# Kernel tuning notes

Measured on AMD Instinct MI355X. Metric: run time of the kernel, lower is better.

Reference implementation:

```python
import jax, jax.numpy as jnp
import numpy as np

N = 100000          # num nodes
E = 1600000         # num edges (before self loops)
IN_C = 128
OUT_C = 64
RATIO = 0.5
NEG_SLOPE = 0.2


def setup_inputs() -> dict:
    key = jax.random.key(0)
    k1, k2, k3, k4, k5 = jax.random.split(key, 5)
    x = jax.random.normal(k1, (N, IN_C), jnp.float32)
    # edges with no self loops (module removes then re-adds self loops)
    src = jax.random.randint(k2, (E,), 0, N, dtype=jnp.int32)
    off = jax.random.randint(k3, (E,), 1, N, dtype=jnp.int32)
    tgt = (src + off) % N
    edge_index = jnp.stack([src, tgt])  # [2, E], row0=source(j), row1=target(i)
    # glorot init
    s_w = float(np.sqrt(6.0 / (IN_C + OUT_C)))
    weight = jax.random.uniform(k4, (IN_C, OUT_C), jnp.float32, -s_w, s_w)
    s_a = float(np.sqrt(6.0 / (1 + 2 * OUT_C)))
    att = jax.random.uniform(k5, (1, 2 * OUT_C), jnp.float32, -s_a, s_a)
    batch = jnp.zeros((N,), jnp.int32)  # single graph
    return {"x": x, "weight": weight, "att": att,
            "edge_index": edge_index, "batch": batch, "bn": 0}


def reference(x, weight, att, edge_index, batch, bn):
    # add self loops (static shapes: E + N edges)
    loops = jnp.arange(N, dtype=edge_index.dtype)
    src = jnp.concatenate([edge_index[0], loops])  # edge_index_j (source)
    tgt = jnp.concatenate([edge_index[1], loops])  # edge_index_i (target)

    h = x @ weight                      # [N, OUT_C]
    x_j = h[src]                        # [E+N, OUT_C] gathered source feats
    x_i = h[tgt]

    # alpha = (cat([x_i, x_j]) * att).sum(-1)
    alpha = x_i @ att[0, :OUT_C] + x_j @ att[0, OUT_C:]   # [E+N]
    alpha = jnp.where(alpha > 0, alpha, NEG_SLOPE * alpha)  # leaky_relu

    # edge-softmax grouped by target node (every node has a self loop -> no empty segment)
    m = jax.ops.segment_max(alpha, tgt, num_segments=N)
    a = jnp.exp(alpha - m[tgt])
    denom = jax.ops.segment_sum(a, tgt, num_segments=N)
    alpha = a / (denom[tgt] + 1e-16)

    # node importance = sum of attention over outgoing edges (grouped by source)
    alpha_sum = jax.ops.segment_sum(alpha, src, num_segments=N)

    # topk node selection (ratio of all nodes; single graph)
    k = int(np.ceil(RATIO * N))
    _, topk_idx = jax.lax.top_k(alpha_sum, k)
    node_mask = jnp.zeros((N,), bool).at[topk_idx].set(True)

    # filter_dn: keep edges whose both endpoints survive; mask instead of compacting
    edge_mask = node_mask[src] & node_mask[tgt]
    alpha_m = jnp.where(edge_mask, alpha, 0.0)

    # weighted scatter-add aggregation to target nodes (aggr='add')
    out = jax.ops.segment_sum(alpha_m[:, None] * x_j, tgt, num_segments=N)  # [N, OUT_C]
    # bn flag is 0 -> BatchNorm skipped
    return out, edge_mask, node_mask
```

## Files before the change

kernel.cpp:

```cpp
#include <hip/hip_runtime.h>
#include <stdint.h>

#define IN_C 128
#define OUT_C 64
#define NEG_SLOPE 0.2f
#define RB 256
#define RBINS 512
#define STAGE 8192
#define NGH (RBINS * RB)
#define NGHS (RBINS * RBINS)
#define KC 8
#define SXW 384

typedef unsigned int u32;
typedef unsigned long long u64;

__device__ __forceinline__ u32 fenc(float f) {
  u32 u = __float_as_uint(f);
  return (u & 0x80000000u) ? ~u : (u | 0x80000000u);
}
__device__ __forceinline__ u64 key64(float v, int i) {
  return (((u64)fenc(v)) << 32) | (u64)(0xffffffffu - (u32)i);
}

__global__ __launch_bounds__(256) void k_gemm(const float* __restrict__ x,
                                              const float* __restrict__ w,
                                              const float* __restrict__ att,
                                              float* __restrict__ h,
                                              float* __restrict__ ai, float* __restrict__ aj,
                                              int N) {
  __shared__ float sw[IN_C * OUT_C];
  __shared__ float sx[KC * SXW];
  int tid = threadIdx.x;
  int rbase = blockIdx.x * 256;

  for (int i = tid; i < (IN_C * OUT_C) / 4; i += 256)
    ((float4*)sw)[i] = ((const float4*)w)[i];

  int c0 = (tid & 7) * 8;
  int rg = tid >> 3;
  int sxbase = rg * 12;
  float acc[8][8];
#pragma unroll
  for (int i = 0; i < 8; i++)
#pragma unroll
    for (int j = 0; j < 8; j++) acc[i][j] = 0.f;

  int str = tid >> 1;
  int skq = tid & 1;

  for (int kb = 0; kb < IN_C; kb += KC) {
    __syncthreads();
#pragma unroll
    for (int it = 0; it < 2; ++it) {
      int r = str + it * 128;
      int grow = rbase + r;
      float4 v = make_float4(0.f, 0.f, 0.f, 0.f);
      if (grow < N) v = *(const float4*)&x[(size_t)grow * IN_C + kb + skq * 4];
      int base = (r >> 3) * 12 + (r & 7);
      sx[(skq * 4 + 0) * SXW + base] = v.x;
      sx[(skq * 4 + 1) * SXW + base] = v.y;
      sx[(skq * 4 + 2) * SXW + base] = v.z;
      sx[(skq * 4 + 3) * SXW + base] = v.w;
    }
    __syncthreads();
#pragma unroll
    for (int kl = 0; kl < KC; ++kl) {
      int kg = kb + kl;
      float xr[8], wv[8];
      *(float4*)&xr[0] = *(const float4*)&sx[kl * SXW + sxbase];
      *(float4*)&xr[4] = *(const float4*)&sx[kl * SXW + sxbase + 4];
      *(float4*)&wv[0] = *(const float4*)&sw[kg * OUT_C + c0];
      *(float4*)&wv[4] = *(const float4*)&sw[kg * OUT_C + c0 + 4];
#pragma unroll
      for (int i = 0; i < 8; ++i)
#pragma unroll
        for (int j = 0; j < 8; ++j)
          acc[i][j] += xr[i] * wv[j];
    }
  }

  float pi[8], pj[8];
#pragma unroll
  for (int i = 0; i < 8; ++i) { pi[i] = 0.f; pj[i] = 0.f; }
#pragma unroll
  for (int j = 0; j < 8; ++j) {
    float a0 = att[c0 + j], a1 = att[OUT_C + c0 + j];
#pragma unroll
    for (int i = 0; i < 8; ++i) {
      pi[i] += acc[i][j] * a0;
      pj[i] += acc[i][j] * a1;
    }
  }
#pragma unroll
  for (int o = 1; o < 8; o <<= 1) {
#pragma unroll
    for (int i = 0; i < 8; ++i) {
      pi[i] += __shfl_xor(pi[i], o);
      pj[i] += __shfl_xor(pj[i], o);
    }
  }
#pragma unroll
  for (int i = 0; i < 8; ++i) {
    int row = rbase + rg * 8 + i;
    if (row < N) {
      *(float4*)&h[(size_t)row * OUT_C + c0]     = make_float4(acc[i][0], acc[i][1], acc[i][2], acc[i][3]);
      *(float4*)&h[(size_t)row * OUT_C + c0 + 4] = make_float4(acc[i][4], acc[i][5], acc[i][6], acc[i][7]);
      if ((tid & 7) == 0) { ai[row] = pi[i]; aj[row] = pj[i]; }
    }
  }
}

__global__ __launch_bounds__(256) void k_rhist_t(const int* __restrict__ tgt,
                                                 int E, int EN, int chunk, u32* __restrict__ gh,
                                                 u32* __restrict__ hist8, u32* __restrict__ done,
                                                 u32* __restrict__ sel, u32* __restrict__ cnt, u32 k) {
  __shared__ u32 lh[RBINS];
  int tid = threadIdx.x, b = blockIdx.x;
  if (b == 0) {
    for (int i = tid; i < 2048; i += 256) hist8[i] = 0u;
    if (tid < 8) { done[tid] = 0u; cnt[tid] = 0u; }
    if (tid == 0) { sel[0] = 0u; sel[1] = 0u; sel[2] = k; sel[3] = 0u; }
  }
  for (int d = tid; d < RBINS; d += 256) lh[d] = 0u;
  __syncthreads();
  int lo = b * chunk, hi = min(lo + chunk, EN);
  for (int e = lo + tid; e < hi; e += 256) {
    int t = (e < E) ? tgt[e] : e - E;
    atomicAdd(&lh[((u32)t) >> 8], 1u);
  }
  __syncthreads();
  for (int d = tid; d < RBINS; d += 256) gh[d * RB + b] = lh[d];
}

__global__ __launch_bounds__(256) void k_scanA(const u32* __restrict__ in, u32* __restrict__ out,
                                               u32* __restrict__ bsum, int n) {
  __shared__ u32 s[256];
  int i = blockIdx.x * 256 + threadIdx.x;
  u32 v = (i < n) ? in[i] : 0u;
  s[threadIdx.x] = v;
  __syncthreads();
  for (int o = 1; o < 256; o <<= 1) {
    u32 t = (threadIdx.x >= (unsigned)o) ? s[threadIdx.x - o] : 0u;
    __syncthreads();
    s[threadIdx.x] += t;
    __syncthreads();
  }
  if (i < n) out[i] = s[threadIdx.x] - v;
  if (threadIdx.x == 255) bsum[blockIdx.x] = s[255];
}

__global__ __launch_bounds__(1024) void k_scanB(u32* __restrict__ bsum, int nb) {
  __shared__ u32 s[1024];
  int tid = threadIdx.x;
  u32 v = (tid < nb) ? bsum[tid] : 0u;
  s[tid] = v;
  __syncthreads();
  for (int o = 1; o < 1024; o <<= 1) {
    u32 t = (tid >= o) ? s[tid - o] : 0u;
    __syncthreads();
    s[tid] += t;
    __syncthreads();
  }
  if (tid < nb) bsum[tid] = s[tid] - v;
}

__global__ __launch_bounds__(256) void k_scanC(u32* __restrict__ out, const u32* __restrict__ bsum, int n) {
  int i = blockIdx.x * 256 + threadIdx.x;
  if (i < n) out[i] += bsum[blockIdx.x];
}

__global__ __launch_bounds__(256) void k_rscatter_t(const int* __restrict__ src, const int* __restrict__ tgt,
                                                    int E, int EN, int chunk,
                                                    const u32* __restrict__ gh, u32* __restrict__ bufB) {
  __shared__ u32 cnt[RBINS];
  int tid = threadIdx.x, b = blockIdx.x;
  for (int d = tid; d < RBINS; d += 256) cnt[d] = gh[d * RB + b];
  __syncthreads();
  int lo = b * chunk, hi = min(lo + chunk, EN);
  for (int e = lo + tid; e < hi; e += 256) {
    int s, t;
    if (e < E) { s = src[e]; t = tgt[e]; } else { s = t = e - E; }
    u32 p = atomicAdd(&cnt[((u32)t) >> 8], 1u);
    bufB[p] = (((u32)t & 255u) << 24) | (u32)s;
  }
}

__global__ __launch_bounds__(256) void k_rpass2(const u32* __restrict__ in, u32* __restrict__ out,
                                                const u32* __restrict__ gh, u32* __restrict__ ghs,
                                                u32* __restrict__ offT,
                                                const float* __restrict__ ai, const float* __restrict__ aj,
                                                float* __restrict__ alpha,
                                                int N, int EN) {
  __shared__ u32 hist[256];
  __shared__ u32 sc[256];
  __shared__ u32 lhs[RBINS];
  __shared__ u32 stage[STAGE];
  int tid = threadIdx.x, d = blockIdx.x;
  u32 start = gh[d * RB];
  u32 end = (d < RBINS - 1) ? gh[(d + 1) * RB] : (u32)EN;
  int sz = (int)(end - start);
  hist[tid] = 0u;
  for (int dd = tid; dd < RBINS; dd += 256) lhs[dd] = 0u;
  __syncthreads();
  for (u32 p = start + tid; p < end; p += 256) {
    u32 it = in[p];
    atomicAdd(&hist[it >> 24], 1u);
    atomicAdd(&lhs[(it & 0xffffffu) >> 8], 1u);
  }
  __syncthreads();
  for (int dd = tid; dd < RBINS; dd += 256) ghs[dd * RBINS + d] = lhs[dd];
  u32 hv = hist[tid];
  sc[tid] = hv;
  __syncthreads();
  for (int o = 1; o < 256; o <<= 1) {
    u32 t = (tid >= o) ? sc[tid - o] : 0u;
    __syncthreads();
    sc[tid] += t;
    __syncthreads();
  }
  u32 excl = sc[tid] - hv;
  int node = (d << 8) + tid;
  if (node < N) offT[node] = start + excl;
  if (node == 0) offT[N] = (u32)EN;
  hist[tid] = excl;
  __syncthreads();
  bool staged = (sz <= STAGE);
  for (u32 p = start + tid; p < end; p += 256) {
    u32 it = in[p];
    u32 lp = atomicAdd(&hist[it >> 24], 1u);
    if (staged) stage[lp] = it;
    else out[start + lp] = it;
  }
  __syncthreads();
  if (staged)
    for (int i = tid; i < sz; i += 256) out[start + i] = stage[i];
  __syncthreads();
  if (node < N) {
    int lb = (tid > 0) ? (int)sc[tid - 1] : 0;
    int le = (int)sc[tid];
    float an = ai[node];
    float mx = -1e30f;
    for (int i = lb; i < le; ++i) {
      u32 it = staged ? stage[i] : out[start + i];
      float a = an + aj[it & 0xffffffu];
      a = a > 0.f ? a : NEG_SLOPE * a;
      mx = fmaxf(mx, a);
      if (staged) stage[i] = __float_as_uint(a);
    }
    float sm = 0.f;
    for (int i = lb; i < le; ++i) {
      float a;
      if (staged) a = __uint_as_float(stage[i]);
      else {
        u32 it = out[start + i];
        a = an + aj[it & 0xffffffu];
        a = a > 0.f ? a : NEG_SLOPE * a;
      }
      float v = expf(a - mx);
      sm += v;
      if (staged) stage[i] = __float_as_uint(v);
      else alpha[start + i] = v;
    }
    float inv = 1.f / (sm + 1e-16f);
    for (int i = lb; i < le; ++i) {
      float v = staged ? __uint_as_float(stage[i]) : alpha[start + i];
      alpha[start + i] = v * inv;
    }
  }
}

__global__ __launch_bounds__(256) void k_rscatter_s(const u32* __restrict__ csr,
                                                    const float* __restrict__ alpha,
                                                    const u32* __restrict__ gh, const u32* __restrict__ ghs,
                                                    u64* __restrict__ bufB, int EN) {
  __shared__ u32 cnt[RBINS];
  int tid = threadIdx.x, d = blockIdx.x;
  for (int dd = tid; dd < RBINS; dd += 256) cnt[dd] = ghs[dd * RBINS + d];
  __syncthreads();
  u32 start = gh[d * RB];
  u32 end = (d < RBINS - 1) ? gh[(d + 1) * RB] : (u32)EN;
  for (u32 e = start + tid; e < end; e += 256) {
    u32 s = csr[e] & 0xffffffu;
    u32 p = atomicAdd(&cnt[s >> 8], 1u);
    bufB[p] = (((u64)(s & 255u)) << 32) | __float_as_uint(alpha[e]);
  }
}

__global__ __launch_bounds__(256) void k_asum_acc(const u64* __restrict__ bufB,
                                                  const u32* __restrict__ ghs,
                                                  float* __restrict__ asum, int N, int EN) {
  __shared__ float sums[256];
  int tid = threadIdx.x, d = blockIdx.x;
  u32 start = ghs[d * RBINS];
  u32 end = (d < RBINS - 1) ? ghs[(d + 1) * RBINS] : (u32)EN;
  sums[tid] = 0.f;
  __syncthreads();
  for (u32 p = start + tid; p < end; p += 256) {
    u64 it = bufB[p];
    atomicAdd(&sums[(u32)(it >> 32)], __uint_as_float((u32)it));
  }
  __syncthreads();
  int node = d * 256 + tid;
  if (node < N) asum[node] = sums[tid];
}

__global__ __launch_bounds__(256) void k_histpick(const float* __restrict__ asum,
                                                  const u32* __restrict__ list_in, const u32* __restrict__ cnt_in,
                                                  u32* __restrict__ list_out, u32* __restrict__ cnt_out,
                                                  u32* __restrict__ hist8, u32* __restrict__ done,
                                                  u32* __restrict__ sel, int N, int pass, int nblk) {
  __shared__ u32 lh[256];
  __shared__ u32 sres;
  __shared__ u32 s[256];
  int tid = threadIdx.x;
  lh[tid] = 0u;
  __syncthreads();
  u64 prefix = ((const u64*)sel)[0];
  int shift = 56 - 8 * pass;
  int n = list_in ? (int)*cnt_in : N;
  int i = blockIdx.x * 256 + tid;
  if (i < n) {
    int idx = list_in ? (int)list_in[i] : i;
    u64 k = key64(asum[idx], idx);
    bool ok = (pass == 0) || ((k >> (shift + 8)) == prefix);
    if (ok) {
      atomicAdd(&lh[(u32)(k >> shift) & 255u], 1u);
      if (list_out) {
        u32 p = atomicAdd(cnt_out, 1u);
        list_out[p] = (u32)idx;
      }
    }
  }
  __syncthreads();
  if (lh[tid]) atomicAdd(&hist8[pass * 256 + tid], lh[tid]);
  __syncthreads();
  if (tid == 0)
    sres = __hip_atomic_fetch_add(&done[pass], 1u, __ATOMIC_ACQ_REL, __HIP_MEMORY_SCOPE_AGENT);
  __syncthreads();
  if (sres == (u32)(nblk - 1)) {
    u32 krem = sel[2];
    u32 hv = __hip_atomic_load(&hist8[pass * 256 + (255 - tid)], __ATOMIC_RELAXED,
                               __HIP_MEMORY_SCOPE_AGENT);
    s[tid] = hv;
    __syncthreads();
    for (int o = 1; o < 256; o <<= 1) {
      u32 t = (tid >= o) ? s[tid - o] : 0u;
      __syncthreads();
      s[tid] += t;
      __syncthreads();
    }
    u32 cum = s[tid], prev = (tid > 0) ? s[tid - 1] : 0u;
    if (cum >= krem && prev < krem) {
      int dsel = 255 - tid;
      ((u64*)sel)[0] = (prefix << 8) | (u64)(u32)dsel;
      sel[2] = krem - prev;
    }
  }
}

__global__ __launch_bounds__(256) void k_finish(const float* __restrict__ asum,
                                                const u32* __restrict__ list, const u32* __restrict__ cntp,
                                                u32* __restrict__ sel) {
  __shared__ u64 keys[2048];
  __shared__ u32 cc;
  int tid = threadIdx.x;
  if (tid == 0) cc = 0u;
  __syncthreads();
  int n = (int)*cntp;
  u32 fsel = (u32)((const u64*)sel)[0];
  u32 krem = sel[2];
  for (int i = tid; i < n; i += 256) {
    int idx = (int)list[i];
    u64 k = key64(asum[idx], idx);
    if ((u32)(k >> 32) == fsel) {
      u32 p = atomicAdd(&cc, 1u);
      if (p < 2048) keys[p] = k;
    }
  }
  __syncthreads();
  int C = (int)min(cc, 2048u);
  for (int i = tid; i < C; i += 256) {
    u64 k = keys[i];
    u32 rank = 0;
    for (int j = 0; j < C; ++j)
      if (keys[j] > k) rank++;
    if (rank == krem - 1) ((u64*)sel)[0] = k;
  }
}

__global__ __launch_bounds__(256) void k_node_mask(const float* __restrict__ asum,
                                                   const u32* __restrict__ sel,
                                                   u32* __restrict__ nm,
                                                   float* __restrict__ out_node, int N) {
  int i = blockIdx.x * 256 + threadIdx.x;
  if (i >= N) return;
  u64 T = ((const u64*)sel)[0];
  bool m = key64(asum[i], i) >= T;
  nm[i] = m ? 1u : 0u;
  out_node[i] = m ? 1.f : 0.f;
}

__global__ __launch_bounds__(256) void k_mask(const int* __restrict__ src, const int* __restrict__ tgt,
                                              const u32* __restrict__ nm,
                                              const u32* __restrict__ csr, const float* __restrict__ alpha,
                                              float* __restrict__ out_edge, u64* __restrict__ pair,
                                              int E, int EN) {
  int e = blockIdx.x * 256 + threadIdx.x;
  if (e >= EN) return;
  int s, t;
  if (e < E) { s = src[e]; t = tgt[e]; } else { s = t = e - E; }
  out_edge[e] = (nm[s] && nm[t]) ? 1.f : 0.f;
  u32 sp = csr[e] & 0xffffffu;
  u32 ab = nm[sp] ? __float_as_uint(alpha[e]) : 0u;
  pair[e] = (((u64)sp) << 32) | ab;
}

__global__ __launch_bounds__(256) void k_aggregate(const u32* __restrict__ off,
                                                   const u64* __restrict__ pair,
                                                   const float* __restrict__ h,
                                                   const u32* __restrict__ nm,
                                                   float* __restrict__ out, int N) {
  int node = blockIdx.x * 4 + (threadIdx.x >> 6);
  int lane = threadIdx.x & 63;
  int g = lane >> 4;
  int c = lane & 15;
  if (node >= N) return;
  float4 acc = make_float4(0.f, 0.f, 0.f, 0.f);
  if (nm[node]) {
    u32 b = off[node], e2 = off[node + 1];
    for (u32 p0 = b; p0 < e2; p0 += 16) {
      u64 pr[4];
      float av[4];
      u32 sv[4];
#pragma unroll
      for (int q = 0; q < 4; ++q) {
        u32 p = p0 + q * 4 + (u32)g;
        bool ok = p < e2;
        pr[q] = pair[ok ? p : b];
        av[q] = ok ? __uint_as_float((u32)pr[q]) : 0.f;
        sv[q] = (u32)(pr[q] >> 32);
      }
      float4 hv[4];
#pragma unroll
      for (int q = 0; q < 4; ++q)
        hv[q] = *(const float4*)&h[(size_t)sv[q] * OUT_C + c * 4];
#pragma unroll
      for (int q = 0; q < 4; ++q) {
        acc.x += av[q] * hv[q].x;
        acc.y += av[q] * hv[q].y;
        acc.z += av[q] * hv[q].z;
        acc.w += av[q] * hv[q].w;
      }
    }
#pragma unroll
    for (int o = 16; o < 64; o <<= 1) {
      acc.x += __shfl_xor(acc.x, o);
      acc.y += __shfl_xor(acc.y, o);
      acc.z += __shfl_xor(acc.z, o);
      acc.w += __shfl_xor(acc.w, o);
    }
  }
  if (g == 0)
    *(float4*)&out[(size_t)node * OUT_C + c * 4] = acc;
}

extern "C" void kernel_launch(void* const* d_in, const int* in_sizes, int n_in,
                              void* d_out, int out_size, void* d_ws, size_t ws_size,
                              hipStream_t stream) {
  const float* x   = (const float*)d_in[0];
  const float* w   = (const float*)d_in[1];
  const float* att = (const float*)d_in[2];
  const int*   ei  = (const int*)d_in[3];

  int N = in_sizes[0] / IN_C;
  int E = in_sizes[3] / 2;
  int EN = E + N;
  const int* src = ei;
  const int* tgt = ei + E;

  float* out      = (float*)d_out;
  float* out_edge = out + (size_t)N * OUT_C;
  float* out_node = out_edge + (size_t)EN;

  char* p = (char*)d_ws;
  auto alloc = [&](size_t bytes) -> char* {
    char* r = p;
    p += (bytes + 255) & ~(size_t)255;
    return r;
  };
  float* h     = (float*)alloc((size_t)N * OUT_C * 4);
  float* ai    = (float*)alloc((size_t)N * 4);
  float* aj    = (float*)alloc((size_t)N * 4);
  u32*   bufA  = (u32*)alloc((size_t)EN * 4);
  u64*   bufB  = (u64*)alloc((size_t)EN * 8);
  float* alpha = (float*)alloc((size_t)EN * 4);
  u32*   offT  = (u32*)alloc((size_t)(N + 1) * 4);
  u32*   gh    = (u32*)alloc((size_t)NGH * 4);
  u32*   ghs   = (u32*)alloc((size_t)NGHS * 4);
  u32*   bsum  = (u32*)alloc(2048 * 4);
  float* asum  = (float*)alloc((size_t)N * 4);
  u32*   nm    = (u32*)alloc((size_t)N * 4);
  u32*   hist8 = (u32*)alloc(2048 * 4);
  u32*   done  = (u32*)alloc(8 * 4);
  u32*   cnt   = (u32*)alloc(8 * 4);
  u32*   sel   = (u32*)alloc(256);
  u32*   listA = (u32*)alloc((size_t)N * 4);
  u32*   listB = (u32*)alloc((size_t)N * 4);

  u32 kSel = (u32)((N + 1) / 2);
  int chunk = (EN + RB - 1) / RB;
  int nScanT = (NGH + 255) / 256;
  int nScanS = (NGHS + 255) / 256;
  int gRow = (N + 255) / 256;
  int gN = (N + 255) / 256;
  int gE = (EN + 255) / 256;
  int gNode4 = (N + 3) / 4;

  k_gemm<<<gRow, 256, 0, stream>>>(x, w, att, h, ai, aj, N);

  k_rhist_t<<<RB, 256, 0, stream>>>(tgt, E, EN, chunk, gh, hist8, done, sel, cnt, kSel);
  k_scanA<<<nScanT, 256, 0, stream>>>(gh, gh, bsum, NGH);
  k_scanB<<<1, 1024, 0, stream>>>(bsum, nScanT);
  k_scanC<<<nScanT, 256, 0, stream>>>(gh, bsum, NGH);
  k_rscatter_t<<<RB, 256, 0, stream>>>(src, tgt, E, EN, chunk, gh, (u32*)bufB);
  k_rpass2<<<RBINS, 256, 0, stream>>>((u32*)bufB, bufA, gh, ghs, offT, ai, aj, alpha, N, EN);

  k_scanA<<<nScanS, 256, 0, stream>>>(ghs, ghs, bsum, NGHS);
  k_scanB<<<1, 1024, 0, stream>>>(bsum, nScanS);
  k_scanC<<<nScanS, 256, 0, stream>>>(ghs, bsum, NGHS);
  k_rscatter_s<<<RBINS, 256, 0, stream>>>(bufA, alpha, gh, ghs, bufB, EN);
  k_asum_acc<<<RBINS, 256, 0, stream>>>(bufB, ghs, asum, N, EN);

  k_histpick<<<gN, 256, 0, stream>>>(asum, nullptr, nullptr, nullptr, nullptr,
                                     hist8, done, sel, N, 0, gN);
  k_histpick<<<gN, 256, 0, stream>>>(asum, nullptr, nullptr, listA, &cnt[1],
                                     hist8, done, sel, N, 1, gN);
  k_histpick<<<gN, 256, 0, stream>>>(asum, listA, &cnt[1], listB, &cnt[2],
                                     hist8, done, sel, N, 2, gN);
  k_histpick<<<gN, 256, 0, stream>>>(asum, listB, &cnt[2], listA, &cnt[3],
                                     hist8, done, sel, N, 3, gN);
  k_finish<<<1, 256, 0, stream>>>(asum, listA, &cnt[3], sel);

  k_node_mask<<<gN, 256, 0, stream>>>(asum, sel, nm, out_node, N);
  k_mask<<<gE, 256, 0, stream>>>(src, tgt, nm, bufA, alpha, out_edge, bufB, E, EN);
  k_aggregate<<<gNode4, 256, 0, stream>>>(offT, bufB, h, nm, out, N);
}
```

Before: 370.5 us.

## Rewrite projection GEMM with register-resident weight columns and per-wave row staging

Replaces the LDS-tiled 8x8 register-blocked GEMM with a scheme where each lane keeps one full weight column (128 floats) in registers. Each wave stages four x rows at a time in shared memory, software-prefetching the next four rows. The attention dot products are now reduced with a 64-lane shuffle tree per row instead of an 8-lane reduction. This removes the shared weight tile and block-wide barriers, but needs many more registers per thread, which lowers occupancy, and does about 12 shuffles per row plus scalar h stores.

```diff
diff --git a/kernel.cpp b/kernel.cpp
--- a/kernel.cpp
+++ b/kernel.cpp
@@ -9,8 +9,6 @@
 #define STAGE 8192
 #define NGH (RBINS * RB)
 #define NGHS (RBINS * RBINS)
-#define KC 8
-#define SXW 384
 
 typedef unsigned int u32;
 typedef unsigned long long u64;
@@ -29,84 +27,76 @@
                                               float* __restrict__ h,
                                               float* __restrict__ ai, float* __restrict__ aj,
                                               int N) {
-  __shared__ float sw[IN_C * OUT_C];
-  __shared__ float sx[KC * SXW];
-  int tid = threadIdx.x;
-  int rbase = blockIdx.x * 256;
-
-  for (int i = tid; i < (IN_C * OUT_C) / 4; i += 256)
-    ((float4*)sw)[i] = ((const float4*)w)[i];
-
-  int c0 = (tid & 7) * 8;
-  int rg = tid >> 3;
-  int sxbase = rg * 12;
-  float acc[8][8];
-#pragma unroll
-  for (int i = 0; i < 8; i++)
-#pragma unroll
-    for (int j = 0; j < 8; j++) acc[i][j] = 0.f;
-
-  int str = tid >> 1;
-  int skq = tid & 1;
-
-  for (int kb = 0; kb < IN_C; kb += KC) {
-    __syncthreads();
-#pragma unroll
-    for (int it = 0; it < 2; ++it) {
-      int r = str + it * 128;
-      int grow = rbase + r;
-      float4 v = make_float4(0.f, 0.f, 0.f, 0.f);
-      if (grow < N) v = *(const float4*)&x[(size_t)grow * IN_C + kb + skq * 4];
-      int base = (r >> 3) * 12 + (r & 7);
-      sx[(skq * 4 + 0) * SXW + base] = v.x;
-      sx[(skq * 4 + 1) * SXW + base] = v.y;
-      sx[(skq * 4 + 2) * SXW + base] = v.z;
-      sx[(skq * 4 + 3) * SXW + base] = v.w;
-    }
-    __syncthreads();
-#pragma unroll
-    for (int kl = 0; kl < KC; ++kl) {
-      int kg = kb + kl;
-      float xr[8], wv[8];
-      *(float4*)&xr[0] = *(const float4*)&sx[kl * SXW + sxbase];
-      *(float4*)&xr[4] = *(const float4*)&sx[kl * SXW + sxbase + 4];
-      *(float4*)&wv[0] = *(const float4*)&sw[kg * OUT_C + c0];
-      *(float4*)&wv[4] = *(const float4*)&sw[kg * OUT_C + c0 + 4];
-#pragma unroll
-      for (int i = 0; i < 8; ++i)
-#pragma unroll
-        for (int j = 0; j < 8; ++j)
-          acc[i][j] += xr[i] * wv[j];
-    }
-  }
-
-  float pi[8], pj[8];
-#pragma unroll
-  for (int i = 0; i < 8; ++i) { pi[i] = 0.f; pj[i] = 0.f; }
-#pragma unroll
-  for (int j = 0; j < 8; ++j) {
-    float a0 = att[c0 + j], a1 = att[OUT_C + c0 + j];
-#pragma unroll
-    for (int i = 0; i < 8; ++i) {
-      pi[i] += acc[i][j] * a0;
-      pj[i] += acc[i][j] * a1;
-    }
-  }
-#pragma unroll
-  for (int o = 1; o < 8; o <<= 1) {
-#pragma unroll
-    for (int i = 0; i < 8; ++i) {
-      pi[i] += __shfl_xor(pi[i], o);
-      pj[i] += __shfl_xor(pj[i], o);
-    }
-  }
-#pragma unroll
-  for (int i = 0; i < 8; ++i) {
-    int row = rbase + rg * 8 + i;
-    if (row < N) {
-      *(float4*)&h[(size_t)row * OUT_C + c0]     = make_float4(acc[i][0], acc[i][1], acc[i][2], acc[i][3]);
-      *(float4*)&h[(size_t)row * OUT_C + c0 + 4] = make_float4(acc[i][4], acc[i][5], acc[i][6], acc[i][7]);
-      if ((tid & 7) == 0) { ai[row] = pi[i]; aj[row] = pj[i]; }
+  __shared__ float sx[4][4 * IN_C];
+  const int tid = threadIdx.x;
+  const int lane = tid & 63;
+  const int wid = tid >> 6;
+  float* sxw = sx[wid];
+
+  float wcol[IN_C];
+#pragma unroll
+  for (int k = 0; k < IN_C; ++k) wcol[k] = w[k * OUT_C + lane];
+
+  const float a0 = att[lane];
+  const float a1 = att[OUT_C + lane];
+
+  const int rw0 = blockIdx.x * 128 + wid * 32;
+
+  const int s0 = lane;
+  const int s1 = lane + 64;
+
+  float4 nva, nvb;
+  {
+    int r0 = rw0 + (s0 >> 5); if (r0 >= N) r0 = N - 1;
+    int r1 = rw0 + (s1 >> 5); if (r1 >= N) r1 = N - 1;
+    nva = *(const float4*)&x[(size_t)r0 * IN_C + (s0 & 31) * 4];
+    nvb = *(const float4*)&x[(size_t)r1 * IN_C + (s1 & 31) * 4];
+  }
+
+  for (int t = 0; t < 8; ++t) {
+    *(float4*)&sxw[s0 * 4] = nva;
+    *(float4*)&sxw[s1 * 4] = nvb;
+    if (t + 1 < 8) {
+      int rb = rw0 + (t + 1) * 4;
+      int r0 = rb + (s0 >> 5); if (r0 >= N) r0 = N - 1;
+      int r1 = rb + (s1 >> 5); if (r1 >= N) r1 = N - 1;
+      nva = *(const float4*)&x[(size_t)r0 * IN_C + (s0 & 31) * 4];
+      nvb = *(const float4*)&x[(size_t)r1 * IN_C + (s1 & 31) * 4];
+    }
+
+    float acc[4];
+    acc[0] = 0.f; acc[1] = 0.f; acc[2] = 0.f; acc[3] = 0.f;
+#pragma unroll
+    for (int kk = 0; kk < IN_C; kk += 4) {
+      float4 x0 = *(const float4*)&sxw[0 * IN_C + kk];
+      float4 x1 = *(const float4*)&sxw[1 * IN_C + kk];
+      float4 x2 = *(const float4*)&sxw[2 * IN_C + kk];
+      float4 x3 = *(const float4*)&sxw[3 * IN_C + kk];
+      acc[0] += x0.x * wcol[kk + 0]; acc[1] += x1.x * wcol[kk + 0];
+      acc[2] += x2.x * wcol[kk + 0]; acc[3] += x3.x * wcol[kk + 0];
+      acc[0] += x0.y * wcol[kk + 1]; acc[1] += x1.y * wcol[kk + 1];
+      acc[2] += x2.y * wcol[kk + 1]; acc[3] += x3.y * wcol[kk + 1];
+      acc[0] += x0.z * wcol[kk + 2]; acc[1] += x1.z * wcol[kk + 2];
+      acc[2] += x2.z * wcol[kk + 2]; acc[3] += x3.z * wcol[kk + 2];
+      acc[0] += x0.w * wcol[kk + 3]; acc[1] += x1.w * wcol[kk + 3];
+      acc[2] += x2.w * wcol[kk + 3]; acc[3] += x3.w * wcol[kk + 3];
+    }
+
+    const int rbase2 = rw0 + t * 4;
+#pragma unroll
+    for (int r = 0; r < 4; ++r) {
+      int row = rbase2 + r;
+      float v = acc[r];
+      float pi = v * a0, pj = v * a1;
+#pragma unroll
+      for (int o = 1; o < 64; o <<= 1) {
+        pi += __shfl_xor(pi, o);
+        pj += __shfl_xor(pj, o);
+      }
+      if (row < N) {
+        h[(size_t)row * OUT_C + lane] = v;
+        if (lane == 0) { ai[row] = pi; aj[row] = pj; }
+      }
     }
   }
 }
@@ -512,12 +502,12 @@
   int chunk = (EN + RB - 1) / RB;
   int nScanT = (NGH + 255) / 256;
   int nScanS = (NGHS + 255) / 256;
-  int gRow = (N + 255) / 256;
+  int gGemm = (N + 127) / 128;
   int gN = (N + 255) / 256;
   int gE = (EN + 255) / 256;
   int gNode4 = (N + 3) / 4;
 
-  k_gemm<<<gRow, 256, 0, stream>>>(x, w, att, h, ai, aj, N);
+  k_gemm<<<gGemm, 256, 0, stream>>>(x, w, att, h, ai, aj, N);
 
   k_rhist_t<<<RB, 256, 0, stream>>>(tgt, E, EN, chunk, gh, hist8, done, sel, cnt, kSel);
   k_scanA<<<nScanT, 256, 0, stream>>>(gh, gh, bsum, NGH);
```

After: 527.6 us. 1.42x slower.

## Halve GEMM block size and register-prefetch next x tile

Applied to the files above, without the earlier changes.

Shrinks the node-feature GEMM block from 256 to 128 rows and threads, so each thread owns one row and loads its 8 k-values as two float4s. The loads for the next k-chunk are issued into registers before the compute loop, overlapping global latency with the FMAs. This doubles the grid and reloads the weight matrix into shared memory twice as often, with per-thread row reads becoming strided rather than coalesced across threads.

```diff
diff --git a/kernel.cpp b/kernel.cpp
--- a/kernel.cpp
+++ b/kernel.cpp
@@ -10,7 +10,7 @@
 #define NGH (RBINS * RB)
 #define NGHS (RBINS * RBINS)
 #define KC 8
-#define SXW 384
+#define SXW 192
 
 typedef unsigned int u32;
 typedef unsigned long long u64;
@@ -23,7 +23,7 @@
   return (((u64)fenc(v)) << 32) | (u64)(0xffffffffu - (u32)i);
 }
 
-__global__ __launch_bounds__(256) void k_gemm(const float* __restrict__ x,
+__global__ __launch_bounds__(128) void k_gemm(const float* __restrict__ x,
                                               const float* __restrict__ w,
                                               const float* __restrict__ att,
                                               float* __restrict__ h,
@@ -32,9 +32,9 @@
   __shared__ float sw[IN_C * OUT_C];
   __shared__ float sx[KC * SXW];
   int tid = threadIdx.x;
-  int rbase = blockIdx.x * 256;
-
-  for (int i = tid; i < (IN_C * OUT_C) / 4; i += 256)
+  int rbase = blockIdx.x * 128;
+
+  for (int i = tid; i < (IN_C * OUT_C) / 4; i += 128)
     ((float4*)sw)[i] = ((const float4*)w)[i];
 
   int c0 = (tid & 7) * 8;
@@ -46,22 +46,30 @@
 #pragma unroll
     for (int j = 0; j < 8; j++) acc[i][j] = 0.f;
 
-  int str = tid >> 1;
-  int skq = tid & 1;
+  int grow = rbase + tid;
+  int base = (tid >> 3) * 12 + (tid & 7);
+  const float* xp = &x[(size_t)grow * IN_C];
+
+  float4 pv0 = make_float4(0.f, 0.f, 0.f, 0.f);
+  float4 pv1 = make_float4(0.f, 0.f, 0.f, 0.f);
+  if (grow < N) {
+    pv0 = *(const float4*)&xp[0];
+    pv1 = *(const float4*)&xp[4];
+  }
 
   for (int kb = 0; kb < IN_C; kb += KC) {
     __syncthreads();
-#pragma unroll
-    for (int it = 0; it < 2; ++it) {
-      int r = str + it * 128;
-      int grow = rbase + r;
-      float4 v = make_float4(0.f, 0.f, 0.f, 0.f);
-      if (grow < N) v = *(const float4*)&x[(size_t)grow * IN_C + kb + skq * 4];
-      int base = (r >> 3) * 12 + (r & 7);
-      sx[(skq * 4 + 0) * SXW + base] = v.x;
-      sx[(skq * 4 + 1) * SXW + base] = v.y;
-      sx[(skq * 4 + 2) * SXW + base] = v.z;
-      sx[(skq * 4 + 3) * SXW + base] = v.w;
+    sx[0 * SXW + base] = pv0.x;
+    sx[1 * SXW + base] = pv0.y;
+    sx[2 * SXW + base] = pv0.z;
+    sx[3 * SXW + base] = pv0.w;
+    sx[4 * SXW + base] = pv1.x;
+    sx[5 * SXW + base] = pv1.y;
+    sx[6 * SXW + base] = pv1.z;
+    sx[7 * SXW + base] = pv1.w;
+    if (kb + KC < IN_C && grow < N) {
+      pv0 = *(const float4*)&xp[kb + KC];
+      pv1 = *(const float4*)&xp[kb + KC + 4];
     }
     __syncthreads();
 #pragma unroll
@@ -512,12 +520,12 @@
   int chunk = (EN + RB - 1) / RB;
   int nScanT = (NGH + 255) / 256;
   int nScanS = (NGHS + 255) / 256;
-  int gRow = (N + 255) / 256;
+  int gGemm = (N + 127) / 128;
   int gN = (N + 255) / 256;
   int gE = (EN + 255) / 256;
   int gNode4 = (N + 3) / 4;
 
-  k_gemm<<<gRow, 256, 0, stream>>>(x, w, att, h, ai, aj, N);
+  k_gemm<<<gGemm, 128, 0, stream>>>(x, w, att, h, ai, aj, N);
 
   k_rhist_t<<<RB, 256, 0, stream>>>(tgt, E, EN, chunk, gh, hist8, done, sel, cnt, kSel);
   k_scanA<<<nScanT, 256, 0, stream>>>(gh, gh, bsum, NGH);
```

After: 365.6 us. About the same (-1.3%).
